# Performance work log

Hardware: AMD Instinct MI355X
Metric: run time of the kernel (lower is better)

Reference implementation:

```python
import jax, jax.numpy as jnp
import numpy as np

GROUPS = [1, 2, 2, 3]

def setup_inputs() -> dict:
    key = jax.random.key(0)
    ks = jax.random.split(key, 8)
    b, dim, h, w = 8, 256, 64, 64
    return {
        "x": jax.random.normal(ks[0], (b, dim, h, w), dtype=jnp.float32),
        "temperature": jnp.ones((4, 1, 1), dtype=jnp.float32),          # nn.Parameter(torch.ones(4,1,1))
        "w_qkv": jax.random.normal(ks[1], (3 * dim, dim)) * 0.02,        # Conv2d(dim,3dim,1,bias=False)
        "w_dw": jax.random.normal(ks[2], (3 * dim, 1, 3, 3)) * 0.1,      # depthwise 3x3, groups=3dim
        "w_proj": jax.random.normal(ks[3], (dim, dim)) * 0.02,           # Conv2d(dim,dim,1,bias=False)
        "w_gate": jax.random.normal(ks[4], (dim, dim)) * 0.02,           # Intra gatingConv (Conv1d k=1)
        "b_gate": jnp.zeros((dim,), dtype=jnp.float32),
        "w_down": jax.random.normal(ks[5], (dim // 2, dim)) * 0.02,      # Intra down
        "b_down": jnp.zeros((dim // 2,), dtype=jnp.float32),
        "w_up": jax.random.normal(ks[6], (dim, dim // 2)) * 0.02,        # Intra up
        "b_up": jnp.zeros((dim,), dtype=jnp.float32),
    }

def _l2norm(t):
    # torch F.normalize(dim=-1): x / max(||x||, 1e-12)
    return t / jnp.maximum(jnp.linalg.norm(t, axis=-1, keepdims=True), 1e-12)

def reference(x, temperature, w_qkv, w_dw, w_proj, w_gate, b_gate, w_down, b_down, w_up, b_up):
    b, c, h, w = x.shape
    L = h * w
    # qkv = dwconv3x3(conv1x1(x))
    qkv = jnp.einsum('bchw,oc->bohw', x, w_qkv)
    qkv = jax.lax.conv_general_dilated(qkv, w_dw, (1, 1), ((1, 1), (1, 1)),
                                       feature_group_count=3 * c,
                                       dimension_numbers=('NCHW', 'OIHW', 'NCHW'))
    q, k, v = jnp.split(qkv, 3, axis=1)
    q = q.reshape(b, c, L); k = k.reshape(b, c, L); v = v.reshape(b, c, L)
    # ReGroup: sort channels by mean activation (descending), split per ratio
    order = jnp.argsort(-q.mean(axis=2).mean(axis=0))
    qs, ks_, vs = q[:, order], k[:, order], v[:, order]
    total = sum(GROUPS)
    sizes = [int(r / total * c) for r in GROUPS]
    sizes[-1] += c - sum(sizes)
    outs, caches = [], []
    start = 0
    for i, g in enumerate(sizes):
        qg = qs[:, start:start + g]; kg = ks_[:, start:start + g]; vg = vs[:, start:start + g]
        start += g
        qn = _l2norm(qg); kn = _l2norm(kg)
        attn = jax.nn.softmax(jnp.einsum('bcl,bdl->bcd', qn, kn) * temperature[i], axis=-1)  # (b,Cg,Cg)
        caches.append(jax.lax.stop_gradient(qn + kn))  # q.detach()+k.detach()
        outs.append(jnp.einsum('bcd,bdl->bcl', attn, vg))
    # CalculateCurrentLayerCache: mean over L, channel-tile to c, bilinear 1x1->sxs == broadcast
    s = int(L ** 0.5 + 0.9999)
    accum = jnp.zeros((b, c), dtype=x.dtype)
    for tc, g in zip(caches, sizes):
        gm = tc.mean(axis=-1)                     # (b, Cg)
        rep = max(1, c // g)
        tiled = jnp.tile(gm, (1, rep))
        if tiled.shape[1] > c:
            tiled = tiled[:, :c]
        elif tiled.shape[1] < c:
            tiled = jnp.pad(tiled, ((0, 0), (0, c - tiled.shape[1])))
        accum = accum + tiled
    accum = accum / len(caches)
    qv_cache = 0.9 * jnp.broadcast_to(accum[:, :, None, None], (b, c, s, s))
    out_all = jnp.concatenate(outs, axis=1)       # (b, c, L)
    tmp_caches = jnp.concatenate(caches, axis=1)  # (b, c, L)
    # Intra_CacheModulation: gated = gelu(gateConv(z)) * z ; out = up(down(gated))
    z = tmp_caches + out_all
    gating = jax.nn.gelu(jnp.einsum('oc,bcl->bol', w_gate, z) + b_gate[None, :, None], approximate=False)
    gated = gating * z
    mid = jnp.einsum('oc,bcl->bol', w_down, gated) + b_down[None, :, None]
    intra = jnp.einsum('oc,bcl->bol', w_up, mid) + b_up[None, :, None]
    out_all = (intra + out_all).reshape(b, c, h, w)
    out_all = jnp.einsum('bchw,oc->bohw', out_all, w_proj)
    return (out_all, qv_cache)
```

## Files before the change

### kernel.cpp

```cpp
#include <hip/hip_runtime.h>
#include <hip/hip_fp16.h>
#include <math.h>

#define B 8
#define C 256
#define L 4096
#define OC3 768

typedef __attribute__((ext_vector_type(8))) short short8v;
typedef __attribute__((ext_vector_type(8))) unsigned short u16x8;
typedef __attribute__((ext_vector_type(4))) float f32x4;

__device__ __forceinline__ float gelu_exact(float x){
  return 0.5f * x * (1.0f + erff(x * 0.70710678118654752440f));
}
__device__ __forceinline__ float wave_sum(float v){
  #pragma unroll
  for (int off = 32; off > 0; off >>= 1) v += __shfl_down(v, off, 64);
  return v;
}
__device__ __forceinline__ unsigned short bf16_rne(float f){
  unsigned int u = __float_as_uint(f);
  unsigned int r = u + 0x7FFFu + ((u >> 16) & 1u);
  return (unsigned short)(r >> 16);
}
__device__ __forceinline__ float bf16_tof(unsigned short h){
  return __uint_as_float(((unsigned int)h) << 16);
}
__device__ __forceinline__ unsigned int splitpack(float v){
  unsigned short hi = bf16_rne(v);
  float lof = v - bf16_tof(hi);
  unsigned short lo = bf16_rne(lof);
  return (unsigned int)hi | ((unsigned int)lo << 16);
}
__device__ __forceinline__ unsigned short f16b(float f){
  return __half_as_ushort(__float2half_rn(f));
}
__device__ __forceinline__ float f16tof(unsigned short u){
  return __half2float(__ushort_as_half(u));
}
__device__ __forceinline__ unsigned int splitpackh(float v){
  unsigned short hi = f16b(v);
  float lof = v - f16tof(hi);
  unsigned short lo = f16b(lof);
  return (unsigned int)hi | ((unsigned int)lo << 16);
}
__device__ __forceinline__ void gl16(const unsigned short* g, unsigned short* l){
  __builtin_amdgcn_global_load_lds(
      (const __attribute__((address_space(1))) void*)g,
      (__attribute__((address_space(3))) void*)l, 16, 0, 0);
}

__global__ __launch_bounds__(256) void wsplit_kernel(
    const float* __restrict__ wqkv, const float* __restrict__ wgate,
    const float* __restrict__ wdown, const float* __restrict__ wup,
    const float* __restrict__ wproj,
    unsigned short* __restrict__ Wf16,
    unsigned short* __restrict__ PH, unsigned short* __restrict__ PLo)
{
  int idx = blockIdx.x * 256 + threadIdx.x;
  if (idx < 327680) {
    float s;
    if (idx < 196608)      s = wqkv[idx];
    else if (idx < 262144) s = wgate[idx - 196608];
    else if (idx < 294912) s = wdown[idx - 262144];
    else                   s = wup[idx - 294912];
    Wf16[idx] = f16b(s);
  } else {
    int j = idx - 327680;
    unsigned int p = splitpack(wproj[j]);
    PH[j] = (unsigned short)(p & 0xFFFFu); PLo[j] = (unsigned short)(p >> 16);
  }
}

__global__ __launch_bounds__(256) void splitx_kernel(const float* __restrict__ x,
    unsigned short* __restrict__ XThi, unsigned short* __restrict__ XTlo)
{
  __shared__ float st[64][68];
  const int b = blockIdx.z, c0 = blockIdx.y * 64, lb = blockIdx.x * 64;
  const int t = threadIdx.x;
  #pragma unroll
  for (int i = 0; i < 4; i++) {
    int row = (t >> 4) + i * 16;
    int col = (t & 15) * 4;
    float4 v = *(const float4*)&x[((size_t)b * C + c0 + row) * L + lb + col];
    st[row][col] = v.x; st[row][col+1] = v.y; st[row][col+2] = v.z; st[row][col+3] = v.w;
  }
  __syncthreads();
  const int l = t >> 2, cq = t & 3;
  u16x8 hv0, hv1, lv0, lv1;
  #pragma unroll
  for (int i = 0; i < 16; i++) {
    unsigned int p = splitpackh(st[cq * 16 + i][l]);
    if (i < 8) { hv0[i] = (unsigned short)(p & 0xFFFFu); lv0[i] = (unsigned short)(p >> 16); }
    else       { hv1[i-8] = (unsigned short)(p & 0xFFFFu); lv1[i-8] = (unsigned short)(p >> 16); }
  }
  size_t o = ((size_t)b * L + lb + l) * C + c0 + cq * 16;
  *(u16x8*)&XThi[o]     = hv0;
  *(u16x8*)&XThi[o + 8] = hv1;
  *(u16x8*)&XTlo[o]     = lv0;
  *(u16x8*)&XTlo[o + 8] = lv1;
}

template<int KTOT, int EPI, int MODE>
__global__ __launch_bounds__(256) void hgemm(
    const unsigned short* __restrict__ Ahi_g, const unsigned short* __restrict__ Alo_g,
    const unsigned short* __restrict__ Bw_g,
    float* __restrict__ outF,
    unsigned short* __restrict__ outH, unsigned short* __restrict__ outLo,
    const float* __restrict__ bias, const unsigned short* __restrict__ extraH,
    int Ntot)
{
  constexpr int NP = (MODE == 1) ? 2 : 3;
  __shared__ unsigned short SB[2][NP][128 * 32];
  const int t  = threadIdx.x;
  const int lb = blockIdx.x * 128;
  const int o0 = blockIdx.y * 128;
  const int b  = blockIdx.z;
  const int w  = t >> 6, lane = t & 63;
  const int wm = w >> 1, wn = w & 1;
  const int ln = lane & 15, lg = lane >> 4;
  const int lrow  = lane >> 2;
  const int chunk = (lane & 3) ^ ((lane >> 4) & 3);
  const int slot  = lg ^ (ln >> 2);
  const bool twop = (MODE == 2) ? (blockIdx.y < 2) : false;

  f32x4 z4 = {0.f, 0.f, 0.f, 0.f};
  f32x4 acc[4][4];
  #pragma unroll
  for (int i = 0; i < 4; i++)
    #pragma unroll
    for (int j = 0; j < 4; j++) acc[i][j] = z4;

  const size_t arow0 = (size_t)b * L + lb;
  constexpr int NKT = KTOT / 32;

  auto stage = [&](int kt, int cb) {
    const int k0 = kt * 32;
    #pragma unroll
    for (int i = 0; i < 2; i++) {
      const int rb = w * 32 + i * 16;
      const size_t ga = (arow0 + rb + lrow) * KTOT + k0 + chunk * 8;
      gl16(Ahi_g + ga, &SB[cb][0][rb * 32]);
      if (NP == 3 && twop) gl16(Alo_g + ga, &SB[cb][1][rb * 32]);
      const size_t gb = (size_t)(o0 + rb + lrow) * KTOT + k0 + chunk * 8;
      gl16(Bw_g + gb, &SB[cb][NP - 1][rb * 32]);
    }
  };

  stage(0, 0);
  __syncthreads();
  int cur = 0;
  for (int kt = 0; kt < NKT; ++kt) {
    if (kt + 1 < NKT) stage(kt + 1, cur ^ 1);
    short8v bwf[4];
    #pragma unroll
    for (int nf = 0; nf < 4; nf++) {
      const int off = (wn * 64 + nf * 16 + ln) * 32 + slot * 8;
      bwf[nf] = *(const short8v*)&SB[cur][NP - 1][off];
    }
    #pragma unroll
    for (int mf = 0; mf < 4; mf++) {
      const int off = (wm * 64 + mf * 16 + ln) * 32 + slot * 8;
      const short8v ah = *(const short8v*)&SB[cur][0][off];
      #pragma unroll
      for (int nf = 0; nf < 4; nf++)
        acc[mf][nf] = __builtin_amdgcn_mfma_f32_16x16x32_f16(ah, bwf[nf], acc[mf][nf], 0, 0, 0);
      if (NP == 3 && twop) {
        const short8v al = *(const short8v*)&SB[cur][1][off];
        #pragma unroll
        for (int nf = 0; nf < 4; nf++)
          acc[mf][nf] = __builtin_amdgcn_mfma_f32_16x16x32_f16(al, bwf[nf], acc[mf][nf], 0, 0, 0);
      }
    }
    __syncthreads();
    cur ^= 1;
  }
  #pragma unroll
  for (int mf = 0; mf < 4; mf++) {
    const int mbase = lb + wm * 64 + mf * 16 + lg * 4;
    #pragma unroll
    for (int nf = 0; nf < 4; nf++) {
      const int o = o0 + wn * 64 + nf * 16 + ln;
      if (EPI == 0) {
        float4 r;
        r.x = acc[mf][nf][0]; r.y = acc[mf][nf][1];
        r.z = acc[mf][nf][2]; r.w = acc[mf][nf][3];
        *(float4*)&outF[((size_t)b * Ntot + o) * L + mbase] = r;
      } else {
        const float bv = bias ? bias[o] : 0.0f;
        #pragma unroll
        for (int r = 0; r < 4; r++) {
          const size_t idx = ((size_t)b * L + mbase + r) * Ntot + o;
          float v = acc[mf][nf][r] + bv;
          if (EPI == 2) { v = gelu_exact(v) * f16tof(extraH[idx]); }
          if (EPI == 5) { v = v + f16tof(extraH[idx]); }
          if (EPI == 5) {
            const unsigned int p = splitpack(v);
            outH[idx]  = (unsigned short)(p & 0xFFFFu);
            outLo[idx] = (unsigned short)(p >> 16);
          } else {
            outH[idx] = f16b(v);
          }
        }
      }
    }
  }
}

template<int KTOT>
__global__ __launch_bounds__(256) void mgemm(
    const unsigned short* __restrict__ Ahi_g, const unsigned short* __restrict__ Alo_g,
    const unsigned short* __restrict__ Bhi_g, const unsigned short* __restrict__ Blo_g,
    float* __restrict__ outF, int Ntot)
{
  __shared__ unsigned short SB[2][4][128 * 32];
  const int t  = threadIdx.x;
  const int lb = blockIdx.x * 128;
  const int o0 = blockIdx.y * 128;
  const int b  = blockIdx.z;
  const int w  = t >> 6, lane = t & 63;
  const int wm = w >> 1, wn = w & 1;
  const int ln = lane & 15, lg = lane >> 4;
  const int lrow  = lane >> 2;
  const int chunk = (lane & 3) ^ ((lane >> 4) & 3);
  const int slot  = lg ^ (ln >> 2);

  f32x4 z4 = {0.f, 0.f, 0.f, 0.f};
  f32x4 acc[4][4];
  #pragma unroll
  for (int i = 0; i < 4; i++)
    #pragma unroll
    for (int j = 0; j < 4; j++) acc[i][j] = z4;

  const size_t arow0 = (size_t)b * L + lb;
  constexpr int NKT = KTOT / 32;

  auto stage = [&](int kt, int cb) {
    const int k0 = kt * 32;
    #pragma unroll
    for (int i = 0; i < 2; i++) {
      const int rb = w * 32 + i * 16;
      const size_t ga = (arow0 + rb + lrow) * KTOT + k0 + chunk * 8;
      gl16(Ahi_g + ga, &SB[cb][0][rb * 32]);
      gl16(Alo_g + ga, &SB[cb][1][rb * 32]);
      const size_t gb = (size_t)(o0 + rb + lrow) * KTOT + k0 + chunk * 8;
      gl16(Bhi_g + gb, &SB[cb][2][rb * 32]);
      gl16(Blo_g + gb, &SB[cb][3][rb * 32]);
    }
  };

  stage(0, 0);
  __syncthreads();
  int cur = 0;
  for (int kt = 0; kt < NKT; ++kt) {
    if (kt + 1 < NKT) stage(kt + 1, cur ^ 1);
    short8v bhf[4], blf[4];
    #pragma unroll
    for (int nf = 0; nf < 4; nf++) {
      const int off = (wn * 64 + nf * 16 + ln) * 32 + slot * 8;
      bhf[nf] = *(const short8v*)&SB[cur][2][off];
      blf[nf] = *(const short8v*)&SB[cur][3][off];
    }
    #pragma unroll
    for (int mf = 0; mf < 4; mf++) {
      const int off = (wm * 64 + mf * 16 + ln) * 32 + slot * 8;
      const short8v ah = *(const short8v*)&SB[cur][0][off];
      const short8v al = *(const short8v*)&SB[cur][1][off];
      #pragma unroll
      for (int nf = 0; nf < 4; nf++) {
        acc[mf][nf] = __builtin_amdgcn_mfma_f32_16x16x32_bf16(ah, bhf[nf], acc[mf][nf], 0, 0, 0);
        acc[mf][nf] = __builtin_amdgcn_mfma_f32_16x16x32_bf16(ah, blf[nf], acc[mf][nf], 0, 0, 0);
        acc[mf][nf] = __builtin_amdgcn_mfma_f32_16x16x32_bf16(al, bhf[nf], acc[mf][nf], 0, 0, 0);
      }
    }
    __syncthreads();
    cur ^= 1;
  }
  #pragma unroll
  for (int mf = 0; mf < 4; mf++) {
    const int mbase = lb + wm * 64 + mf * 16 + lg * 4;
    #pragma unroll
    for (int nf = 0; nf < 4; nf++) {
      const int o = o0 + wn * 64 + nf * 16 + ln;
      float4 r;
      r.x = acc[mf][nf][0]; r.y = acc[mf][nf][1];
      r.z = acc[mf][nf][2]; r.w = acc[mf][nf][3];
      *(float4*)&outF[((size_t)b * Ntot + o) * L + mbase] = r;
    }
  }
}

__global__ __launch_bounds__(256) void dwconv2_kernel(
    const float* __restrict__ in, const float* __restrict__ wdw,
    unsigned short* __restrict__ qkF, unsigned short* __restrict__ vF,
    float* __restrict__ csum, float* __restrict__ csumsq)
{
  __shared__ float p[66][73];
  __shared__ float rs[4][2];
  const int ch = blockIdx.x;
  const int b  = blockIdx.y;
  const int t  = threadIdx.x;
  const size_t base = ((size_t)b * OC3 + ch) * L;
  float wt[9];
  #pragma unroll
  for (int j = 0; j < 9; j++) wt[j] = wdw[ch * 9 + j];
  if (t < 66) { p[0][3 + t] = 0.f; p[65][3 + t] = 0.f; }
  if (t < 64) { p[1 + t][3] = 0.f; p[1 + t][68] = 0.f; }
  #pragma unroll
  for (int i = 0; i < 4; i++) {
    int pix = (i * 256 + t) * 4;
    const float4 v = *reinterpret_cast<const float4*>(&in[base + pix]);
    int h = pix >> 6, ww = pix & 63;
    p[1+h][4+ww] = v.x; p[1+h][5+ww] = v.y; p[1+h][6+ww] = v.z; p[1+h][7+ww] = v.w;
  }
  __syncthreads();
  const int h  = t >> 2;
  const int w0 = (t & 3) * 16;
  float r0a[18], r1a[18], r2a[18];
  #pragma unroll
  for (int c = 0; c < 18; c++) {
    r0a[c] = p[h][w0 + 3 + c];
    r1a[c] = p[h + 1][w0 + 3 + c];
    r2a[c] = p[h + 2][w0 + 3 + c];
  }
  float res[16];
  float s = 0.f, s2 = 0.f;
  #pragma unroll
  for (int j = 0; j < 16; j++) {
    float acc;
    acc = r0a[j] * wt[0];
    acc = fmaf(r0a[j+1], wt[1], acc);
    acc = fmaf(r0a[j+2], wt[2], acc);
    acc = fmaf(r1a[j],   wt[3], acc);
    acc = fmaf(r1a[j+1], wt[4], acc);
    acc = fmaf(r1a[j+2], wt[5], acc);
    acc = fmaf(r2a[j],   wt[6], acc);
    acc = fmaf(r2a[j+1], wt[7], acc);
    acc = fmaf(r2a[j+2], wt[8], acc);
    res[j] = acc;
    s += acc;
    s2 = fmaf(acc, acc, s2);
  }
  u16x8 h0, h1;
  #pragma unroll
  for (int j = 0; j < 16; j++) {
    if (j < 8) h0[j]   = f16b(res[j]);
    else       h1[j-8] = f16b(res[j]);
  }
  if (ch < 512) {
    const size_t qi = ((size_t)b * 512 + ch) * L + t * 16;
    *(u16x8*)&qkF[qi]     = h0;
    *(u16x8*)&qkF[qi + 8] = h1;
    s = wave_sum(s); s2 = wave_sum(s2);
    const int lane = t & 63, wid = t >> 6;
    if (lane == 0) { rs[wid][0] = s; rs[wid][1] = s2; }
    __syncthreads();
    if (t == 0) {
      csum[b * 512 + ch]   = rs[0][0] + rs[1][0] + rs[2][0] + rs[3][0];
      csumsq[b * 512 + ch] = rs[0][1] + rs[1][1] + rs[2][1] + rs[3][1];
    }
  } else {
    const size_t vi = ((size_t)b * 256 + (ch - 512)) * L + t * 16;
    *(u16x8*)&vF[vi]     = h0;
    *(u16x8*)&vF[vi + 8] = h1;
  }
}

__global__ __launch_bounds__(256) void rankstats_kernel(
    const float* __restrict__ csum, const float* __restrict__ csumsq,
    int* __restrict__ order,
    float* __restrict__ sumq, float* __restrict__ sumk,
    float* __restrict__ invnq, float* __restrict__ invnk)
{
  const int c = threadIdx.x;
  float key = 0.f;
  #pragma unroll
  for (int b = 0; b < 8; b++) key += csum[b * 512 + c];
  __shared__ float keys[256];
  __shared__ int ordS[256];
  keys[c] = key;
  __syncthreads();
  int rank = 0;
  for (int j = 0; j < 256; j++) {
    float kj = keys[j];
    rank += (kj > key) || (kj == key && j < c);
  }
  order[rank] = c;
  ordS[rank] = c;
  __syncthreads();
  const int ch = ordS[c];
  #pragma unroll
  for (int b = 0; b < 8; b++) {
    sumq[b * 256 + c]  = csum[b * 512 + ch];
    invnq[b * 256 + c] = 1.0f / fmaxf(sqrtf(csumsq[b * 512 + ch]), 1e-12f);
    sumk[b * 256 + c]  = csum[b * 512 + 256 + ch];
    invnk[b * 256 + c] = 1.0f / fmaxf(sqrtf(csumsq[b * 512 + 256 + ch]), 1e-12f);
  }
}

__global__ __launch_bounds__(256) void vpack_kernel(
    const unsigned short* __restrict__ vF, const unsigned short* __restrict__ qkF,
    const int* __restrict__ order,
    const float* __restrict__ invnq, const float* __restrict__ invnk,
    unsigned short* __restrict__ vTS, unsigned short* __restrict__ zqT)
{
  __shared__ float vt[64][65];
  __shared__ float zt[64][65];
  __shared__ int   ordS[256];
  __shared__ float iqS[256], ikS[256];
  const int t = threadIdx.x, lb = blockIdx.x * 64, b = blockIdx.y;
  ordS[t] = order[t];
  iqS[t] = invnq[b * 256 + t];
  ikS[t] = invnk[b * 256 + t];
  __syncthreads();
  for (int cc = 0; cc < 4; cc++) {
    const int r0 = cc * 64;
    for (int i = t; i < 1024; i += 256) {
      const int row = i >> 4, q = i & 15;
      const int ch = ordS[r0 + row];
      const float iq = iqS[r0 + row], ik = ikS[r0 + row];
      const ushort4 v4 = *(const ushort4*)&vF[((size_t)b * 256 + ch) * L + lb + q * 4];
      vt[q*4+0][row] = f16tof(v4.x); vt[q*4+1][row] = f16tof(v4.y);
      vt[q*4+2][row] = f16tof(v4.z); vt[q*4+3][row] = f16tof(v4.w);
      const ushort4 q4 = *(const ushort4*)&qkF[((size_t)b * 512 + ch) * L + lb + q * 4];
      const ushort4 k4 = *(const ushort4*)&qkF[((size_t)b * 512 + 256 + ch) * L + lb + q * 4];
      zt[q*4+0][row] = f16tof(q4.x) * iq + f16tof(k4.x) * ik;
      zt[q*4+1][row] = f16tof(q4.y) * iq + f16tof(k4.y) * ik;
      zt[q*4+2][row] = f16tof(q4.z) * iq + f16tof(k4.z) * ik;
      zt[q*4+3][row] = f16tof(q4.w) * iq + f16tof(k4.w) * ik;
    }
    __syncthreads();
    const int l = t >> 2, qq = t & 3;
    const size_t ob = ((size_t)b * L + lb + l) * 256 + r0 + qq * 16;
    u16x8 vv[2], zz[2];
    #pragma unroll
    for (int j = 0; j < 16; j++) {
      vv[j>>3][j&7] = f16b(vt[l][qq*16 + j]);
      zz[j>>3][j&7] = f16b(zt[l][qq*16 + j]);
    }
    *(u16x8*)&vTS[ob]     = vv[0]; *(u16x8*)&vTS[ob + 8] = vv[1];
    *(u16x8*)&zqT[ob]     = zz[0]; *(u16x8*)&zqT[ob + 8] = zz[1];
    __syncthreads();
  }
}

template<int G, int GI, int START, int MB, int SPB>
__device__ void scores_body(const unsigned short* __restrict__ qkF,
    const int* __restrict__ order, float* __restrict__ Spart,
    unsigned short* Ah, unsigned short* Bh, int* ordS)
{
  constexpr int MR = (G - MB * 64 < 64) ? (G - MB * 64) : 64;
  constexpr int NF = G / 16;
  const int t = threadIdx.x, ks = blockIdx.x, b = blockIdx.y;
  const int w = t >> 6, lane = t & 63, ln = lane & 15, lg = lane >> 4;
  const int lrow  = lane >> 2;
  const int chunk = (lane & 3) ^ ((lane >> 4) & 3);
  const int slot  = lg ^ (ln >> 2);
  for (int i = t; i < G; i += 256) ordS[i] = order[START + i];
  __syncthreads();
  const int k0 = ks * 512;
  const bool act = (w * 16) < MR;
  f32x4 z4 = {0.f, 0.f, 0.f, 0.f};
  f32x4 acc[NF];
  #pragma unroll
  for (int i = 0; i < NF; i++) acc[i] = z4;

  auto stage = [&](int kc, int cb) {
    for (int i = w; i < MR / 16; i += 4) {
      const int rb = i * 16;
      const int ch = ordS[MB * 64 + rb + lrow];
      const size_t g = ((size_t)b * 512 + ch) * L + k0 + kc + chunk * 8;
      gl16(qkF + g, &Ah[cb * 2048 + rb * 32]);
    }
    for (int i = w; i < G / 16; i += 4) {
      const int rb = i * 16;
      const int ch = 256 + ordS[rb + lrow];
      const size_t g = ((size_t)b * 512 + ch) * L + k0 + kc + chunk * 8;
      gl16(qkF + g, &Bh[cb * 3072 + rb * 32]);
    }
  };

  stage(0, 0);
  __syncthreads();
  int cur = 0;
  for (int kc = 0; kc < 512; kc += 32) {
    if (kc + 32 < 512) stage(kc + 32, cur ^ 1);
    if (act) {
      const int aoff = cur * 2048 + (w * 16 + ln) * 32 + slot * 8;
      const short8v ah = *(const short8v*)&Ah[aoff];
      #pragma unroll
      for (int nf = 0; nf < NF; nf++) {
        const int boff = cur * 3072 + (nf * 16 + ln) * 32 + slot * 8;
        const short8v bh = *(const short8v*)&Bh[boff];
        acc[nf] = __builtin_amdgcn_mfma_f32_16x16x32_f16(ah, bh, acc[nf], 0, 0, 0);
      }
    }
    __syncthreads();
    cur ^= 1;
  }
  if (act) {
    float* dst = Spart + (size_t)b * 147456 + SPB + ks * G * G;
    #pragma unroll
    for (int nf = 0; nf < NF; nf++) {
      const int d = nf * 16 + ln;
      #pragma unroll
      for (int r = 0; r < 4; r++) {
        const int m = MB * 64 + w * 16 + lg * 4 + r;
        dst[m * G + d] = acc[nf][r];
      }
    }
  }
}

__global__ __launch_bounds__(256) void scores_kernel(const unsigned short* __restrict__ qkF,
    const int* __restrict__ order, float* __restrict__ Spart)
{
  __shared__ unsigned short Ah[2 * 64 * 32];
  __shared__ unsigned short Bh[2 * 96 * 32];
  __shared__ int ordS[96];
  switch (blockIdx.z) {
    case 0:  scores_body<32, 0, 0,   0, 0    >(qkF, order, Spart, Ah, Bh, ordS); break;
    case 1:  scores_body<64, 1, 32,  0, 8192 >(qkF, order, Spart, Ah, Bh, ordS); break;
    case 2:  scores_body<64, 2, 96,  0, 40960>(qkF, order, Spart, Ah, Bh, ordS); break;
    case 3:  scores_body<96, 3, 160, 0, 73728>(qkF, order, Spart, Ah, Bh, ordS); break;
    default: scores_body<96, 3, 160, 1, 73728>(qkF, order, Spart, Ah, Bh, ordS); break;
  }
}

template<int G, int GI, int START, int SPB, int AOFF>
__device__ void softmax_body(const float* __restrict__ Spart, const float* __restrict__ invnq,
    const float* __restrict__ invnk, const float* __restrict__ temperature,
    unsigned short* __restrict__ attnP, float* Sm)
{
  constexpr int RQ = G / 4;
  const int t = threadIdx.x;
  const int b = blockIdx.x;
  const int r0 = blockIdx.z * RQ;
  const float temp = temperature[GI];
  for (int idx = t; idx < RQ * G; idx += 256) {
    const int rl = idx / G, d = idx - rl * G;
    const int gidx = (r0 + rl) * G + d;
    float s = 0.f;
    #pragma unroll
    for (int ks = 0; ks < 8; ks++)
      s += Spart[(size_t)b * 147456 + SPB + ks * G * G + gidx];
    Sm[idx] = s * invnq[b * 256 + START + r0 + rl] * invnk[b * 256 + START + d] * temp;
  }
  __syncthreads();
  const int wv = t >> 6, lane = t & 63;
  for (int r = wv; r < RQ; r += 4) {
    const float v0 = (lane < G) ? Sm[r * G + lane] : -INFINITY;
    const float v1 = (64 + lane < G) ? Sm[r * G + 64 + lane] : -INFINITY;
    float m = fmaxf(v0, v1);
    #pragma unroll
    for (int off = 32; off > 0; off >>= 1) m = fmaxf(m, __shfl_xor(m, off, 64));
    const float e0 = (lane < G) ? expf(v0 - m) : 0.f;
    const float e1 = (64 + lane < G) ? expf(v1 - m) : 0.f;
    float s = e0 + e1;
    #pragma unroll
    for (int off = 32; off > 0; off >>= 1) s += __shfl_xor(s, off, 64);
    const float inv = 1.0f / s;
    const size_t base = (size_t)b * 18432 + AOFF + (size_t)(r0 + r) * G;
    if (lane < G)      attnP[base + lane]      = f16b(e0 * inv);
    if (64 + lane < G) attnP[base + 64 + lane] = f16b(e1 * inv);
  }
}

__global__ __launch_bounds__(256) void softmax_kernel(const float* __restrict__ Spart,
    const float* __restrict__ invnq, const float* __restrict__ invnk,
    const float* __restrict__ temperature, unsigned short* __restrict__ attnP)
{
  extern __shared__ float smem[];
  switch (blockIdx.y) {
    case 0:  softmax_body<32, 0, 0,   0,     0   >(Spart, invnq, invnk, temperature, attnP, smem); break;
    case 1:  softmax_body<64, 1, 32,  8192,  1024>(Spart, invnq, invnk, temperature, attnP, smem); break;
    case 2:  softmax_body<64, 2, 96,  40960, 5120>(Spart, invnq, invnk, temperature, attnP, smem); break;
    default: softmax_body<96, 3, 160, 73728, 9216>(Spart, invnq, invnk, temperature, attnP, smem); break;
  }
}

template<int G, int GI, int START, int AOFF>
__device__ void pv_body(
    const unsigned short* __restrict__ vTS, const unsigned short* __restrict__ attnP,
    const unsigned short* __restrict__ zqT,
    unsigned short* __restrict__ outT, unsigned short* __restrict__ zT,
    unsigned short* Ah, unsigned short* Bh)
{
  constexpr int NF = G / 16;
  const int t = threadIdx.x, b = blockIdx.y, l0 = blockIdx.x * 128;
  const int w = t >> 6, lane = t & 63, ln = lane & 15, lg = lane >> 4;
  const int lrow  = lane >> 2;
  const int chunk = (lane & 3) ^ ((lane >> 4) & 3);
  const int slot  = lg ^ (ln >> 2);
  f32x4 z4 = {0.f, 0.f, 0.f, 0.f};
  f32x4 acc[2][NF];
  #pragma unroll
  for (int i = 0; i < 2; i++)
    #pragma unroll
    for (int j = 0; j < NF; j++) acc[i][j] = z4;
  for (int kc = 0; kc < G; kc += 32) {
    #pragma unroll
    for (int i = 0; i < 2; i++) {
      const int rb = w * 32 + i * 16;
      const size_t g = ((size_t)b * L + l0 + rb + lrow) * 256 + START + kc + chunk * 8;
      gl16(vTS + g, &Ah[rb * 32]);
    }
    for (int i = w; i < G / 16; i += 4) {
      const int rb = i * 16;
      const size_t g = (size_t)b * 18432 + AOFF + (size_t)(rb + lrow) * G + kc + chunk * 8;
      gl16(attnP + g, &Bh[rb * 32]);
    }
    __syncthreads();
    short8v bhf[NF];
    #pragma unroll
    for (int nf = 0; nf < NF; nf++)
      bhf[nf] = *(const short8v*)&Bh[(nf * 16 + ln) * 32 + slot * 8];
    #pragma unroll
    for (int mi = 0; mi < 2; mi++) {
      const int aoff = ((w * 2 + mi) * 16 + ln) * 32 + slot * 8;
      const short8v ah = *(const short8v*)&Ah[aoff];
      #pragma unroll
      for (int nf = 0; nf < NF; nf++)
        acc[mi][nf] = __builtin_amdgcn_mfma_f32_16x16x32_f16(ah, bhf[nf], acc[mi][nf], 0, 0, 0);
    }
    __syncthreads();
  }
  #pragma unroll
  for (int mi = 0; mi < 2; mi++) {
    const int lbase = l0 + (w * 2 + mi) * 16 + lg * 4;
    #pragma unroll
    for (int nf = 0; nf < NF; nf++) {
      const int col = START + nf * 16 + ln;
      #pragma unroll
      for (int r = 0; r < 4; r++) {
        const size_t idx = ((size_t)b * L + lbase + r) * 256 + col;
        const float v = acc[mi][nf][r];
        outT[idx] = f16b(v);
        zT[idx]   = f16b(v + f16tof(zqT[idx]));
      }
    }
  }
}

__global__ __launch_bounds__(256) void pv_kernel(
    const unsigned short* __restrict__ vTS, const unsigned short* __restrict__ attnP,
    const unsigned short* __restrict__ zqT,
    unsigned short* __restrict__ outT, unsigned short* __restrict__ zT)
{
  __shared__ unsigned short Ah[128 * 32];
  __shared__ unsigned short Bh[96 * 32];
  switch (blockIdx.z) {
    case 0:  pv_body<32, 0, 0,   0   >(vTS, attnP, zqT, outT, zT, Ah, Bh); break;
    case 1:  pv_body<64, 1, 32,  1024>(vTS, attnP, zqT, outT, zT, Ah, Bh); break;
    case 2:  pv_body<64, 2, 96,  5120>(vTS, attnP, zqT, outT, zT, Ah, Bh); break;
    default: pv_body<96, 3, 160, 9216>(vTS, attnP, zqT, outT, zT, Ah, Bh); break;
  }
}

__global__ __launch_bounds__(256) void qv_kernel(const float* __restrict__ sumq,
    const float* __restrict__ sumk, const float* __restrict__ invnq,
    const float* __restrict__ invnk, float* __restrict__ out2)
{
  const int b = blockIdx.x >> 8, r = blockIdx.x & 255;
  float val = 0.f;
  {
    const int idx = b * 256 + 0 + (r & 31);
    val += fmaf(sumq[idx], invnq[idx], sumk[idx] * invnk[idx]);
  }
  {
    const int idx = b * 256 + 32 + (r & 63);
    val += fmaf(sumq[idx], invnq[idx], sumk[idx] * invnk[idx]);
  }
  {
    const int idx = b * 256 + 96 + (r & 63);
    val += fmaf(sumq[idx], invnq[idx], sumk[idx] * invnk[idx]);
  }
  if (r < 192) {
    const int rm = (r < 96) ? r : r - 96;
    const int idx = b * 256 + 160 + rm;
    val += fmaf(sumq[idx], invnq[idx], sumk[idx] * invnk[idx]);
  }
  val *= (1.0f / 4096.f) * 0.25f * 0.9f;
  const float4 o = {val, val, val, val};
  float4* dst = reinterpret_cast<float4*>(out2 + ((size_t)b * C + r) * L);
  for (int i = threadIdx.x; i < 1024; i += 256) dst[i] = o;
}

extern "C" void kernel_launch(void* const* d_in, const int* in_sizes, int n_in,
                              void* d_out, int out_size, void* d_ws, size_t ws_size,
                              hipStream_t stream)
{
  const float* x           = (const float*)d_in[0];
  const float* temperature = (const float*)d_in[1];
  const float* w_qkv       = (const float*)d_in[2];
  const float* w_dw        = (const float*)d_in[3];
  const float* w_proj      = (const float*)d_in[4];
  const float* w_gate      = (const float*)d_in[5];
  const float* b_gate      = (const float*)d_in[6];
  const float* w_down      = (const float*)d_in[7];
  const float* b_down      = (const float*)d_in[8];
  const float* w_up        = (const float*)d_in[9];
  const float* b_up        = (const float*)d_in[10];

  if (ws_size < 202548224ULL) return;

  char* ws = (char*)d_ws;
  float*          qkv_pre  = (float*)(ws);
  unsigned short* vTS      = (unsigned short*)(ws);
  unsigned short* zqT      = (unsigned short*)(ws + 16777216);
  float*          Spart    = (float*)(ws + 33554432);
  unsigned short* attnP    = (unsigned short*)(ws + 38797312);
  unsigned short* preprojh = (unsigned short*)(ws);
  unsigned short* preprojl = (unsigned short*)(ws + 16777216);
  unsigned short* XThi     = (unsigned short*)(ws + 100663296);
  unsigned short* XTlo     = (unsigned short*)(ws + 117440512);
  unsigned short* qkF      = (unsigned short*)(ws + 100663296);
  unsigned short* vF       = (unsigned short*)(ws + 134217728);
  unsigned short* outT     = (unsigned short*)(ws + 150994944);
  unsigned short* zT       = (unsigned short*)(ws + 167772160);
  unsigned short* gated    = (unsigned short*)(ws + 184549376);
  unsigned short* mid      = (unsigned short*)(ws + 100663296);
  unsigned short* Wf16   = (unsigned short*)(ws + 201326592);
  unsigned short* WprojH = (unsigned short*)(ws + 201981952);
  unsigned short* WprojL = (unsigned short*)(ws + 202113024);
  float* csum   = (float*)(ws + 202244096);
  float* csumsq = (float*)(ws + 202260480);
  float* sumq   = (float*)(ws + 202276864);
  float* sumk   = (float*)(ws + 202285056);
  float* invnq  = (float*)(ws + 202293248);
  float* invnk  = (float*)(ws + 202301440);
  int*   order  = (int*)(ws + 202309632);

  float* out_all = (float*)d_out;
  float* qv_out  = out_all + (size_t)B * C * L;

  wsplit_kernel<<<1536, 256, 0, stream>>>(w_qkv, w_gate, w_down, w_up, w_proj,
                                          Wf16, WprojH, WprojL);
  splitx_kernel<<<dim3(64, 4, 8), 256, 0, stream>>>(x, XThi, XTlo);
  hgemm<256, 0, 2><<<dim3(32, 6, 8), 256, 0, stream>>>(
      XThi, XTlo, Wf16, qkv_pre, nullptr, nullptr, nullptr, nullptr, 768);
  dwconv2_kernel<<<dim3(768, 8), 256, 0, stream>>>(qkv_pre, w_dw, qkF, vF, csum, csumsq);
  rankstats_kernel<<<1, 256, 0, stream>>>(csum, csumsq, order, sumq, sumk, invnq, invnk);
  vpack_kernel<<<dim3(64, 8), 256, 0, stream>>>(vF, qkF, order, invnq, invnk, vTS, zqT);
  scores_kernel<<<dim3(8, 8, 5), 256, 0, stream>>>(qkF, order, Spart);
  softmax_kernel<<<dim3(8, 4, 4), 256, 9216, stream>>>(Spart, invnq, invnk, temperature, attnP);
  pv_kernel<<<dim3(32, 8, 4), 256, 0, stream>>>(vTS, attnP, zqT, outT, zT);
  hgemm<256, 2, 1><<<dim3(32, 2, 8), 256, 0, stream>>>(
      zT, nullptr, Wf16 + 196608, nullptr, gated, nullptr, b_gate, zT, 256);
  hgemm<256, 1, 1><<<dim3(32, 1, 8), 256, 0, stream>>>(
      gated, nullptr, Wf16 + 262144, nullptr, mid, nullptr, b_down, nullptr, 128);
  hgemm<128, 5, 1><<<dim3(32, 2, 8), 256, 0, stream>>>(
      mid, nullptr, Wf16 + 294912, nullptr, preprojh, preprojl, b_up, outT, 256);
  mgemm<256><<<dim3(32, 2, 8), 256, 0, stream>>>(
      preprojh, preprojl, WprojH, WprojL, out_all, 256);
  qv_kernel<<<2048, 256, 0, stream>>>(sumq, sumk, invnq, invnk, qv_out);
}
```

Measured before the change: 238.6 us.

## Store K/V projections as fp16 and cut final projection GEMM passes

The QKV GEMM epilogue now writes only the Q third as fp32 and the K/V thirds as fp16. The depthwise conv reads fp16 for those channels, which halves that intermediate traffic. The pre-projection activation is stored as a single fp16 plane rather than a hi/lo split. The final projection runs through a new hgemm mode with two MFMA passes (A times weight-hi plus A times weight-lo) instead of three bf16 passes, with the weight split changed to fp16 hi/lo. This lowers memory traffic and MFMA work, at the cost of reduced precision on K/V and the pre-projection activations.

```diff
diff --git a/kernel.cpp b/kernel.cpp
--- a/kernel.cpp
+++ b/kernel.cpp
@@ -68,8 +68,10 @@
     Wf16[idx] = f16b(s);
   } else {
     int j = idx - 327680;
-    unsigned int p = splitpack(wproj[j]);
-    PH[j] = (unsigned short)(p & 0xFFFFu); PLo[j] = (unsigned short)(p >> 16);
+    float wv = wproj[j];
+    unsigned short hh = f16b(wv);
+    PH[j]  = hh;
+    PLo[j] = f16b(wv - f16tof(hh));
   }
 }
 
@@ -107,7 +109,7 @@
     const unsigned short* __restrict__ Ahi_g, const unsigned short* __restrict__ Alo_g,
     const unsigned short* __restrict__ Bw_g,
     float* __restrict__ outF,
-    unsigned short* __restrict__ outH, unsigned short* __restrict__ outLo,
+    unsigned short* __restrict__ outH,
     const float* __restrict__ bias, const unsigned short* __restrict__ extraH,
     int Ntot)
 {
@@ -142,9 +144,14 @@
       const int rb = w * 32 + i * 16;
       const size_t ga = (arow0 + rb + lrow) * KTOT + k0 + chunk * 8;
       gl16(Ahi_g + ga, &SB[cb][0][rb * 32]);
-      if (NP == 3 && twop) gl16(Alo_g + ga, &SB[cb][1][rb * 32]);
+      if (MODE == 2 && twop) gl16(Alo_g + ga, &SB[cb][1][rb * 32]);
       const size_t gb = (size_t)(o0 + rb + lrow) * KTOT + k0 + chunk * 8;
-      gl16(Bw_g + gb, &SB[cb][NP - 1][rb * 32]);
+      if (MODE == 3) {
+        gl16(Bw_g + gb,  &SB[cb][1][rb * 32]);
+        gl16(Alo_g + gb, &SB[cb][2][rb * 32]);
+      } else {
+        gl16(Bw_g + gb, &SB[cb][NP - 1][rb * 32]);
+      }
     }
   };
 
@@ -153,24 +160,46 @@
   int cur = 0;
   for (int kt = 0; kt < NKT; ++kt) {
     if (kt + 1 < NKT) stage(kt + 1, cur ^ 1);
-    short8v bwf[4];
-    #pragma unroll
-    for (int nf = 0; nf < 4; nf++) {
-      const int off = (wn * 64 + nf * 16 + ln) * 32 + slot * 8;
-      bwf[nf] = *(const short8v*)&SB[cur][NP - 1][off];
-    }
-    #pragma unroll
-    for (int mf = 0; mf < 4; mf++) {
-      const int off = (wm * 64 + mf * 16 + ln) * 32 + slot * 8;
-      const short8v ah = *(const short8v*)&SB[cur][0][off];
+    if (MODE == 3) {
+      short8v bh[4], bl[4];
       #pragma unroll
-      for (int nf = 0; nf < 4; nf++)
-        acc[mf][nf] = __builtin_amdgcn_mfma_f32_16x16x32_f16(ah, bwf[nf], acc[mf][nf], 0, 0, 0);
-      if (NP == 3 && twop) {
-        const short8v al = *(const short8v*)&SB[cur][1][off];
+      for (int nf = 0; nf < 4; nf++) {
+        const int off = (wn * 64 + nf * 16 + ln) * 32 + slot * 8;
+        bh[nf] = *(const short8v*)&SB[cur][1][off];
+        bl[nf] = *(const short8v*)&SB[cur][2][off];
+      }
+      #pragma unroll
+      for (int mf = 0; mf < 4; mf++) {
+        const int off = (wm * 64 + mf * 16 + ln) * 32 + slot * 8;
+        const short8v a = *(const short8v*)&SB[cur][0][off];
+        #pragma unroll
+        for (int nf = 0; nf < 4; nf++) {
+          acc[mf][nf] = __builtin_amdgcn_mfma_f32_16x16x32_f16(a, bh[nf], acc[mf][nf], 0, 0, 0);
+          acc[mf][nf] = __builtin_amdgcn_mfma_f32_16x16x32_f16(a, bl[nf], acc[mf][nf], 0, 0, 0);
+        }
+      }
+    } else {
+      short8v bwf[4];
+      #pragma unroll
+      for (int nf = 0; nf < 4; nf++) {
+        const int off = (wn * 64 + nf * 16 + ln) * 32 + slot * 8;
+        bwf[nf] = *(const short8v*)&SB[cur][NP - 1][off];
+      }
+      #pragma unroll
+      for (int mf = 0; mf < 4; mf++) {
+        const int off = (wm * 64 + mf * 16 + ln) * 32 + slot * 8;
+        const short8v ah = *(const short8v*)&SB[cur][0][off];
         #pragma unroll
         for (int nf = 0; nf < 4; nf++)
-          acc[mf][nf] = __builtin_amdgcn_mfma_f32_16x16x32_f16(al, bwf[nf], acc[mf][nf], 0, 0, 0);
+          acc[mf][nf] = __builtin_amdgcn_mfma_f32_16x16x32_f16(ah, bwf[nf], acc[mf][nf], 0, 0, 0);
+        if (MODE == 2) {
+          if (twop) {
+            const short8v al = *(const short8v*)&SB[cur][1][off];
+            #pragma unroll
+            for (int nf = 0; nf < 4; nf++)
+              acc[mf][nf] = __builtin_amdgcn_mfma_f32_16x16x32_f16(al, bwf[nf], acc[mf][nf], 0, 0, 0);
+          }
+        }
       }
     }
     __syncthreads();
@@ -187,6 +216,18 @@
         r.x = acc[mf][nf][0]; r.y = acc[mf][nf][1];
         r.z = acc[mf][nf][2]; r.w = acc[mf][nf][3];
         *(float4*)&outF[((size_t)b * Ntot + o) * L + mbase] = r;
+      } else if (EPI == 6) {
+        if (o0 < 256) {
+          float4 r;
+          r.x = acc[mf][nf][0]; r.y = acc[mf][nf][1];
+          r.z = acc[mf][nf][2]; r.w = acc[mf][nf][3];
+          *(float4*)&outF[((size_t)b * 256 + o) * L + mbase] = r;
+        } else {
+          ushort4 r;
+          r.x = f16b(acc[mf][nf][0]); r.y = f16b(acc[mf][nf][1]);
+          r.z = f16b(acc[mf][nf][2]); r.w = f16b(acc[mf][nf][3]);
+          *(ushort4*)&outH[((size_t)b * 512 + (o - 256)) * L + mbase] = r;
+        }
       } else {
         const float bv = bias ? bias[o] : 0.0f;
         #pragma unroll
@@ -195,104 +236,16 @@
           float v = acc[mf][nf][r] + bv;
           if (EPI == 2) { v = gelu_exact(v) * f16tof(extraH[idx]); }
           if (EPI == 5) { v = v + f16tof(extraH[idx]); }
-          if (EPI == 5) {
-            const unsigned int p = splitpack(v);
-            outH[idx]  = (unsigned short)(p & 0xFFFFu);
-            outLo[idx] = (unsigned short)(p >> 16);
-          } else {
-            outH[idx] = f16b(v);
-          }
+          outH[idx] = f16b(v);
         }
       }
     }
   }
 }
 
-template<int KTOT>
-__global__ __launch_bounds__(256) void mgemm(
-    const unsigned short* __restrict__ Ahi_g, const unsigned short* __restrict__ Alo_g,
-    const unsigned short* __restrict__ Bhi_g, const unsigned short* __restrict__ Blo_g,
-    float* __restrict__ outF, int Ntot)
-{
-  __shared__ unsigned short SB[2][4][128 * 32];
-  const int t  = threadIdx.x;
-  const int lb = blockIdx.x * 128;
-  const int o0 = blockIdx.y * 128;
-  const int b  = blockIdx.z;
-  const int w  = t >> 6, lane = t & 63;
-  const int wm = w >> 1, wn = w & 1;
-  const int ln = lane & 15, lg = lane >> 4;
-  const int lrow  = lane >> 2;
-  const int chunk = (lane & 3) ^ ((lane >> 4) & 3);
-  const int slot  = lg ^ (ln >> 2);
-
-  f32x4 z4 = {0.f, 0.f, 0.f, 0.f};
-  f32x4 acc[4][4];
-  #pragma unroll
-  for (int i = 0; i < 4; i++)
-    #pragma unroll
-    for (int j = 0; j < 4; j++) acc[i][j] = z4;
-
-  const size_t arow0 = (size_t)b * L + lb;
-  constexpr int NKT = KTOT / 32;
-
-  auto stage = [&](int kt, int cb) {
-    const int k0 = kt * 32;
-    #pragma unroll
-    for (int i = 0; i < 2; i++) {
-      const int rb = w * 32 + i * 16;
-      const size_t ga = (arow0 + rb + lrow) * KTOT + k0 + chunk * 8;
-      gl16(Ahi_g + ga, &SB[cb][0][rb * 32]);
-      gl16(Alo_g + ga, &SB[cb][1][rb * 32]);
-      const size_t gb = (size_t)(o0 + rb + lrow) * KTOT + k0 + chunk * 8;
-      gl16(Bhi_g + gb, &SB[cb][2][rb * 32]);
-      gl16(Blo_g + gb, &SB[cb][3][rb * 32]);
-    }
-  };
-
-  stage(0, 0);
-  __syncthreads();
-  int cur = 0;
-  for (int kt = 0; kt < NKT; ++kt) {
-    if (kt + 1 < NKT) stage(kt + 1, cur ^ 1);
-    short8v bhf[4], blf[4];
-    #pragma unroll
-    for (int nf = 0; nf < 4; nf++) {
-      const int off = (wn * 64 + nf * 16 + ln) * 32 + slot * 8;
-      bhf[nf] = *(const short8v*)&SB[cur][2][off];
-      blf[nf] = *(const short8v*)&SB[cur][3][off];
-    }
-    #pragma unroll
-    for (int mf = 0; mf < 4; mf++) {
-      const int off = (wm * 64 + mf * 16 + ln) * 32 + slot * 8;
-      const short8v ah = *(const short8v*)&SB[cur][0][off];
-      const short8v al = *(const short8v*)&SB[cur][1][off];
-      #pragma unroll
-      for (int nf = 0; nf < 4; nf++) {
-        acc[mf][nf] = __builtin_amdgcn_mfma_f32_16x16x32_bf16(ah, bhf[nf], acc[mf][nf], 0, 0, 0);
-        acc[mf][nf] = __builtin_amdgcn_mfma_f32_16x16x32_bf16(ah, blf[nf], acc[mf][nf], 0, 0, 0);
-        acc[mf][nf] = __builtin_amdgcn_mfma_f32_16x16x32_bf16(al, bhf[nf], acc[mf][nf], 0, 0, 0);
-      }
-    }
-    __syncthreads();
-    cur ^= 1;
-  }
-  #pragma unroll
-  for (int mf = 0; mf < 4; mf++) {
-    const int mbase = lb + wm * 64 + mf * 16 + lg * 4;
-    #pragma unroll
-    for (int nf = 0; nf < 4; nf++) {
-      const int o = o0 + wn * 64 + nf * 16 + ln;
-      float4 r;
-      r.x = acc[mf][nf][0]; r.y = acc[mf][nf][1];
-      r.z = acc[mf][nf][2]; r.w = acc[mf][nf][3];
-      *(float4*)&outF[((size_t)b * Ntot + o) * L + mbase] = r;
-    }
-  }
-}
-
 __global__ __launch_bounds__(256) void dwconv2_kernel(
-    const float* __restrict__ in, const float* __restrict__ wdw,
+    const float* __restrict__ inQ, const unsigned short* __restrict__ inKV,
+    const float* __restrict__ wdw,
     unsigned short* __restrict__ qkF, unsigned short* __restrict__ vF,
     float* __restrict__ csum, float* __restrict__ csumsq)
 {
@@ -301,18 +254,30 @@
   const int ch = blockIdx.x;
   const int b  = blockIdx.y;
   const int t  = threadIdx.x;
-  const size_t base = ((size_t)b * OC3 + ch) * L;
   float wt[9];
   #pragma unroll
   for (int j = 0; j < 9; j++) wt[j] = wdw[ch * 9 + j];
   if (t < 66) { p[0][3 + t] = 0.f; p[65][3 + t] = 0.f; }
   if (t < 64) { p[1 + t][3] = 0.f; p[1 + t][68] = 0.f; }
-  #pragma unroll
-  for (int i = 0; i < 4; i++) {
-    int pix = (i * 256 + t) * 4;
-    const float4 v = *reinterpret_cast<const float4*>(&in[base + pix]);
-    int h = pix >> 6, ww = pix & 63;
-    p[1+h][4+ww] = v.x; p[1+h][5+ww] = v.y; p[1+h][6+ww] = v.z; p[1+h][7+ww] = v.w;
+  if (ch < 256) {
+    const size_t base = ((size_t)b * 256 + ch) * L;
+    #pragma unroll
+    for (int i = 0; i < 4; i++) {
+      int pix = (i * 256 + t) * 4;
+      const float4 v = *reinterpret_cast<const float4*>(&inQ[base + pix]);
+      int h = pix >> 6, ww = pix & 63;
+      p[1+h][4+ww] = v.x; p[1+h][5+ww] = v.y; p[1+h][6+ww] = v.z; p[1+h][7+ww] = v.w;
+    }
+  } else {
+    const size_t base = ((size_t)b * 512 + (ch - 256)) * L + t * 16;
+    const u16x8 a0 = *(const u16x8*)&inKV[base];
+    const u16x8 a1 = *(const u16x8*)&inKV[base + 8];
+    const int h = t >> 2, w0 = (t & 3) * 16;
+    #pragma unroll
+    for (int j = 0; j < 8; j++) {
+      p[1+h][4+w0+j]   = f16tof((unsigned short)a0[j]);
+      p[1+h][12+w0+j]  = f16tof((unsigned short)a1[j]);
+    }
   }
   __syncthreads();
   const int h  = t >> 2;
@@ -706,21 +671,21 @@
   if (ws_size < 202548224ULL) return;
 
   char* ws = (char*)d_ws;
-  float*          qkv_pre  = (float*)(ws);
-  unsigned short* vTS      = (unsigned short*)(ws);
-  unsigned short* zqT      = (unsigned short*)(ws + 16777216);
-  float*          Spart    = (float*)(ws + 33554432);
-  unsigned short* attnP    = (unsigned short*)(ws + 38797312);
-  unsigned short* preprojh = (unsigned short*)(ws);
-  unsigned short* preprojl = (unsigned short*)(ws + 16777216);
-  unsigned short* XThi     = (unsigned short*)(ws + 100663296);
-  unsigned short* XTlo     = (unsigned short*)(ws + 117440512);
-  unsigned short* qkF      = (unsigned short*)(ws + 100663296);
-  unsigned short* vF       = (unsigned short*)(ws + 134217728);
-  unsigned short* outT     = (unsigned short*)(ws + 150994944);
-  unsigned short* zT       = (unsigned short*)(ws + 167772160);
-  unsigned short* gated    = (unsigned short*)(ws + 184549376);
-  unsigned short* mid      = (unsigned short*)(ws + 100663296);
+  float*          qkvQ    = (float*)(ws);
+  unsigned short* kvF     = (unsigned short*)(ws + 33554432);
+  unsigned short* vTS     = (unsigned short*)(ws);
+  unsigned short* zqT     = (unsigned short*)(ws + 16777216);
+  float*          Spart   = (float*)(ws + 33554432);
+  unsigned short* attnP   = (unsigned short*)(ws + 38797312);
+  unsigned short* preproj = (unsigned short*)(ws);
+  unsigned short* XThi    = (unsigned short*)(ws + 100663296);
+  unsigned short* XTlo    = (unsigned short*)(ws + 117440512);
+  unsigned short* qkF     = (unsigned short*)(ws + 100663296);
+  unsigned short* vF      = (unsigned short*)(ws + 134217728);
+  unsigned short* outT    = (unsigned short*)(ws + 150994944);
+  unsigned short* zT      = (unsigned short*)(ws + 167772160);
+  unsigned short* gated   = (unsigned short*)(ws + 184549376);
+  unsigned short* mid     = (unsigned short*)(ws + 100663296);
   unsigned short* Wf16   = (unsigned short*)(ws + 201326592);
   unsigned short* WprojH = (unsigned short*)(ws + 201981952);
   unsigned short* WprojL = (unsigned short*)(ws + 202113024);
@@ -738,21 +703,21 @@
   wsplit_kernel<<<1536, 256, 0, stream>>>(w_qkv, w_gate, w_down, w_up, w_proj,
                                           Wf16, WprojH, WprojL);
   splitx_kernel<<<dim3(64, 4, 8), 256, 0, stream>>>(x, XThi, XTlo);
-  hgemm<256, 0, 2><<<dim3(32, 6, 8), 256, 0, stream>>>(
-      XThi, XTlo, Wf16, qkv_pre, nullptr, nullptr, nullptr, nullptr, 768);
-  dwconv2_kernel<<<dim3(768, 8), 256, 0, stream>>>(qkv_pre, w_dw, qkF, vF, csum, csumsq);
+  hgemm<256, 6, 2><<<dim3(32, 6, 8), 256, 0, stream>>>(
+      XThi, XTlo, Wf16, qkvQ, kvF, nullptr, nullptr, 768);
+  dwconv2_kernel<<<dim3(768, 8), 256, 0, stream>>>(qkvQ, kvF, w_dw, qkF, vF, csum, csumsq);
   rankstats_kernel<<<1, 256, 0, stream>>>(csum, csumsq, order, sumq, sumk, invnq, invnk);
   vpack_kernel<<<dim3(64, 8), 256, 0, stream>>>(vF, qkF, order, invnq, invnk, vTS, zqT);
   scores_kernel<<<dim3(8, 8, 5), 256, 0, stream>>>(qkF, order, Spart);
   softmax_kernel<<<dim3(8, 4, 4), 256, 9216, stream>>>(Spart, invnq, invnk, temperature, attnP);
   pv_kernel<<<dim3(32, 8, 4), 256, 0, stream>>>(vTS, attnP, zqT, outT, zT);
   hgemm<256, 2, 1><<<dim3(32, 2, 8), 256, 0, stream>>>(
-      zT, nullptr, Wf16 + 196608, nullptr, gated, nullptr, b_gate, zT, 256);
+      zT, nullptr, Wf16 + 196608, nullptr, gated, b_gate, zT, 256);
   hgemm<256, 1, 1><<<dim3(32, 1, 8), 256, 0, stream>>>(
-      gated, nullptr, Wf16 + 262144, nullptr, mid, nullptr, b_down, nullptr, 128);
+      gated, nullptr, Wf16 + 262144, nullptr, mid, b_down, nullptr, 128);
   hgemm<128, 5, 1><<<dim3(32, 2, 8), 256, 0, stream>>>(
-      mid, nullptr, Wf16 + 294912, nullptr, preprojh, preprojl, b_up, outT, 256);
-  mgemm<256><<<dim3(32, 2, 8), 256, 0, stream>>>(
-      preprojh, preprojl, WprojH, WprojL, out_all, 256);
+      mid, nullptr, Wf16 + 294912, nullptr, preproj, b_up, outT, 256);
+  hgemm<256, 0, 3><<<dim3(32, 2, 8), 256, 0, stream>>>(
+      preproj, WprojL, WprojH, out_all, nullptr, nullptr, nullptr, 256);
   qv_kernel<<<2048, 256, 0, stream>>>(sumq, sumk, invnq, invnk, qv_out);
 }
```

Measured after the change: 219.3 us. 1.09x faster.
